# Performance work log

Hardware: AMD Instinct MI355X
Metric: run time of the kernel (lower is better)

Reference implementation:

```python
import jax, jax.numpy as jnp
import numpy as np

N, C, E = 100000, 128, 1600000


def setup_inputs() -> dict:
    key = jax.random.key(0)
    ks = jax.random.split(key, 7)
    s = 1.0 / np.sqrt(C)
    return {
        "x": jax.random.normal(ks[0], (N, C), jnp.float32),
        "edge_index": jax.random.randint(ks[1], (2, E), 0, N),
        "weight": jax.random.uniform(ks[2], (C, C), jnp.float32, -s, s),   # GCN weight (evolved)
        "w_ih": jax.random.uniform(ks[3], (4 * C, C), jnp.float32, -s, s),  # LSTM input weights
        "w_hh": jax.random.uniform(ks[4], (4 * C, C), jnp.float32, -s, s),  # LSTM hidden weights (h0=0 -> no fwd effect)
        "b_ih": jax.random.uniform(ks[5], (4 * C,), jnp.float32, -s, s),
        "b_hh": jax.random.uniform(ks[6], (4 * C,), jnp.float32, -s, s),
    }


def reference(x, edge_index, weight, w_ih, w_hh, b_ih, b_hh):
    n = x.shape[0]
    # --- LSTM single step over the weight matrix (seq=1, batch=C, h0=c0=0) ---
    # h0 = 0 so w_hh contributes nothing to the forward pass.
    gates = weight @ w_ih.T + b_ih + b_hh  # [C, 4C]
    i, f, g, o = jnp.split(gates, 4, axis=1)
    c = jax.nn.sigmoid(i) * jnp.tanh(g)           # f-gate * c0 = 0
    w_new = jax.nn.sigmoid(o) * jnp.tanh(c)       # evolved GCN weight [C, C]
    del w_hh  # zero forward contribution, kept for faithfulness

    xw = x @ w_new  # [N, C]
    loop = jnp.arange(n)
    src = jnp.concatenate([edge_index[0], loop])  # source j
    dst = jnp.concatenate([edge_index[1], loop])  # target i
    ew = jnp.ones(src.shape[0], x.dtype)          # edge_weight defaults to 1 (improved=False -> self-loop weight 1)
    deg = jax.ops.segment_sum(ew, dst, num_segments=n)
    dinv = jnp.where(deg > 0, jax.lax.rsqrt(jnp.maximum(deg, 1e-12)), 0.0)
    norm = dinv[src] * dinv[dst]                  # [E+N]
    # gather messages, scale, scatter-add to targets
    return jax.ops.segment_sum(xw[src] * norm[:, None], dst, num_segments=n)
```

## Files before the change

### kernel.cpp

```cpp
#include <hip/hip_runtime.h>
#include <hip/hip_bf16.h>
#include <math.h>

typedef __hip_bfloat16  bf16_t;
typedef __attribute__((ext_vector_type(8))) short  short8;
typedef __attribute__((ext_vector_type(4))) float  f32x4;
typedef __attribute__((ext_vector_type(4))) int    intv4;

#define CDIM 128
#define KCAP 32

static __device__ __forceinline__ float sigm(float x){ return 1.0f/(1.0f+__expf(-x)); }
static __device__ __forceinline__ float bflo(unsigned u){ return __builtin_bit_cast(float, u << 16); }
static __device__ __forceinline__ float bfhi(unsigned u){ return __builtin_bit_cast(float, u & 0xffff0000u); }
static __device__ __forceinline__ unsigned short f2bf_u(float f){
    __hip_bfloat16 h = __float2bfloat16(f);
    return __builtin_bit_cast(unsigned short, h);
}
static __device__ __forceinline__ unsigned packbf(float a, float b){
    return (unsigned)f2bf_u(a) | ((unsigned)f2bf_u(b) << 16);
}
static __device__ __forceinline__ short f2bf_s(float f){
    return (short)f2bf_u(f);
}

__global__ void k_lstm(const float* __restrict__ weight, const float* __restrict__ w_ih,
                       const float* __restrict__ b_ih,   const float* __restrict__ b_hh,
                       short* __restrict__ wfrag, int* __restrict__ zptr, int zcount){
    const int gtid = blockIdx.x*CDIM + threadIdx.x;
    for(int i = gtid; i < zcount; i += CDIM*CDIM) zptr[i] = 0;

    __shared__ float wrow[CDIM];
    const int r = blockIdx.x, j = threadIdx.x;
    wrow[j] = weight[r*CDIM + j];
    __syncthreads();
    const float4* wi = (const float4*)(w_ih + (size_t)j*CDIM);
    const float4* wg = (const float4*)(w_ih + (size_t)(2*CDIM + j)*CDIM);
    const float4* wo = (const float4*)(w_ih + (size_t)(3*CDIM + j)*CDIM);
    const float4* wr = (const float4*)wrow;
    float si = 0.f, sg = 0.f, so = 0.f;
    #pragma unroll 8
    for(int k = 0; k < CDIM/4; k++){
        float4 w4 = wr[k];
        float4 a = wi[k]; si += w4.x*a.x + w4.y*a.y + w4.z*a.z + w4.w*a.w;
        float4 b = wg[k]; sg += w4.x*b.x + w4.y*b.y + w4.z*b.z + w4.w*b.w;
        float4 c = wo[k]; so += w4.x*c.x + w4.y*c.y + w4.z*c.z + w4.w*c.w;
    }
    si += b_ih[j]        + b_hh[j];
    sg += b_ih[2*CDIM+j] + b_hh[2*CDIM+j];
    so += b_ih[3*CDIM+j] + b_hh[3*CDIM+j];
    float c  = sigm(si)*tanhf(sg);
    float wv = sigm(so)*tanhf(c);
    const int t = r >> 5, quad = (r >> 3) & 3, jj = r & 7;
    const int n0 = j >> 4, mm = j & 15;
    wfrag[((size_t)((t*8 + n0)*64 + quad*16 + mm))*8 + jj] = f2bf_s(wv);
}

__global__ __launch_bounds__(256) void k_fillcast(const int* __restrict__ src, const int* __restrict__ dst,
        int e, int* __restrict__ cnt, int* __restrict__ csr,
        int2* __restrict__ spill, int* __restrict__ spillc, int nper,
        const float* __restrict__ x, bf16_t* __restrict__ y0, int nf4,
        int castblocks, int edgeblocks){
    if((int)blockIdx.x < castblocks){
        const float4* xv = (const float4*)x;
        uint2* yv = (uint2*)y0;
        const int t0   = blockIdx.x*256 + threadIdx.x;
        const int step = castblocks*256;
        for(int i = t0; i < nf4; i += step){
            float4 v = xv[i];
            uint2 o; o.x = packbf(v.x, v.y); o.y = packbf(v.z, v.w);
            yv[i] = o;
        }
        return;
    }
    const int bid = (int)blockIdx.x - castblocks;
    const int grp = bid & 7;
    const int lo  = grp*nper, hi = lo + nper;
    const int tid = (bid >> 3)*256 + threadIdx.x;
    const int nt  = (edgeblocks >> 3)*256;
    const int e4  = e >> 2;
    const intv4* d4 = (const intv4*)dst;
    const intv4* s4 = (const intv4*)src;
    for(int i = tid; i < e4; i += nt){
        intv4 d = __builtin_nontemporal_load(d4 + i);
        intv4 s = __builtin_nontemporal_load(s4 + i);
        #pragma unroll
        for(int c = 0; c < 4; c++){
            int di = d[c];
            if(di >= lo && di < hi){
                int p = atomicAdd(&cnt[di], 1);
                if(p < KCAP) csr[(size_t)di*KCAP + p] = s[c];
                else { int sp = atomicAdd(spillc, 1); spill[sp] = make_int2(s[c], di); }
            }
        }
    }
    for(int k = e4*4 + tid; k < e; k += nt){
        int di = dst[k];
        if(di >= lo && di < hi){
            int sv = src[k];
            int p = atomicAdd(&cnt[di], 1);
            if(p < KCAP) csr[(size_t)di*KCAP + p] = sv;
            else { int sp = atomicAdd(spillc, 1); spill[sp] = make_int2(sv, di); }
        }
    }
}

__global__ __launch_bounds__(256) void k_agg(const bf16_t* __restrict__ y, const int* __restrict__ csr,
                      const int* __restrict__ deg, const int2* __restrict__ spill,
                      const int* __restrict__ spillc, bf16_t* __restrict__ agg, int n){
    const int node = (int)(((size_t)blockIdx.x*256 + threadIdx.x) >> 6);
    if(node >= n) return;
    const int lane = threadIdx.x & 63;
    const int q = lane >> 4, f = lane & 15;
    const int   cnt = deg[node];
    const float di  = rsqrtf((float)(cnt + 1));
    const int   m   = cnt < KCAP ? cnt : KCAP;
    const uint4* yrow = (const uint4*)y;
    uint4 sv = yrow[(size_t)node*16 + f];
    int jid = (lane < m) ? csr[(size_t)node*KCAP + lane] : 0;

    int jv[8];
    #pragma unroll
    for(int t = 0; t < 8; t++) jv[t] = __shfl(jid, 4*t + q, 64);

    int dgv[8];
    #pragma unroll
    for(int t = 0; t < 8; t++)
        if(4*t + q < m) dgv[t] = deg[jv[t]];

    uint4 v[8];
    #pragma unroll
    for(int t = 0; t < 8; t++)
        if(4*t + q < m) v[t] = yrow[(size_t)jv[t]*16 + f];

    float acc[8];
    #pragma unroll
    for(int i = 0; i < 8; i++) acc[i] = 0.f;
    #pragma unroll
    for(int t = 0; t < 8; t++){
        if(4*t + q < m){
            float dj = rsqrtf((float)(dgv[t] + 1));
            acc[0] += dj*bflo(v[t].x); acc[1] += dj*bfhi(v[t].x);
            acc[2] += dj*bflo(v[t].y); acc[3] += dj*bfhi(v[t].y);
            acc[4] += dj*bflo(v[t].z); acc[5] += dj*bfhi(v[t].z);
            acc[6] += dj*bflo(v[t].w); acc[7] += dj*bfhi(v[t].w);
        }
    }
    int sc = *spillc;
    if(sc > 0){
        for(int t = q; t < sc; t += 4){
            int2 sd = spill[t];
            if(sd.y == node){
                float dj = rsqrtf((float)(deg[sd.x] + 1));
                uint4 vv = yrow[(size_t)sd.x*16 + f];
                acc[0] += dj*bflo(vv.x); acc[1] += dj*bfhi(vv.x);
                acc[2] += dj*bflo(vv.y); acc[3] += dj*bfhi(vv.y);
                acc[4] += dj*bflo(vv.z); acc[5] += dj*bfhi(vv.z);
                acc[6] += dj*bflo(vv.w); acc[7] += dj*bfhi(vv.w);
            }
        }
    }
    #pragma unroll
    for(int i = 0; i < 8; i++){
        acc[i] += __shfl_xor(acc[i], 16, 64);
        acc[i] += __shfl_xor(acc[i], 32, 64);
    }
    if(q == 0){
        uint4 o;
        o.x = packbf(di*(acc[0] + di*bflo(sv.x)), di*(acc[1] + di*bfhi(sv.x)));
        o.y = packbf(di*(acc[2] + di*bflo(sv.y)), di*(acc[3] + di*bfhi(sv.y)));
        o.z = packbf(di*(acc[4] + di*bflo(sv.z)), di*(acc[5] + di*bfhi(sv.z)));
        o.w = packbf(di*(acc[6] + di*bflo(sv.w)), di*(acc[7] + di*bfhi(sv.w)));
        ((uint4*)agg)[(size_t)node*16 + f] = o;
    }
}

__global__ __launch_bounds__(256) void k_mgemm(const bf16_t* __restrict__ agg,
                                               const short* __restrict__ wfrag,
                                               float* __restrict__ out, int n){
    const int wid  = blockIdx.x*4 + (threadIdx.x >> 6);
    const int row0 = wid*16;
    if(row0 >= n) return;
    const int lane = threadIdx.x & 63;
    const int m    = lane & 15, quad = lane >> 4;
    int arow = row0 + m; if(arow > n-1) arow = n-1;
    const short* ap = (const short*)agg + (size_t)arow*CDIM + quad*8;
    short8 a0 = *(const short8*)(ap);
    short8 a1 = *(const short8*)(ap + 32);
    short8 a2 = *(const short8*)(ap + 64);
    short8 a3 = *(const short8*)(ap + 96);
    const short8* bp = (const short8*)wfrag;
    float* orow = out + (size_t)(row0 + quad*4)*CDIM + m;
    const bool full = (row0 + 16 <= n);
    #pragma unroll
    for(int n0 = 0; n0 < 8; n0++){
        f32x4 acc = {0.f, 0.f, 0.f, 0.f};
        acc = __builtin_amdgcn_mfma_f32_16x16x32_bf16(a0, bp[(0*8+n0)*64 + lane], acc, 0, 0, 0);
        acc = __builtin_amdgcn_mfma_f32_16x16x32_bf16(a1, bp[(1*8+n0)*64 + lane], acc, 0, 0, 0);
        acc = __builtin_amdgcn_mfma_f32_16x16x32_bf16(a2, bp[(2*8+n0)*64 + lane], acc, 0, 0, 0);
        acc = __builtin_amdgcn_mfma_f32_16x16x32_bf16(a3, bp[(3*8+n0)*64 + lane], acc, 0, 0, 0);
        if(full){
            #pragma unroll
            for(int r = 0; r < 4; r++)
                orow[(size_t)r*CDIM + n0*16] = acc[r];
        } else {
            #pragma unroll
            for(int r = 0; r < 4; r++)
                if(row0 + quad*4 + r < n) orow[(size_t)r*CDIM + n0*16] = acc[r];
        }
    }
}

extern "C" void kernel_launch(void* const* d_in, const int* in_sizes, int n_in,
                              void* d_out, int out_size, void* d_ws, size_t ws_size,
                              hipStream_t stream){
    const float* x      = (const float*)d_in[0];
    const int*   ei     = (const int*)  d_in[1];
    const float* weight = (const float*)d_in[2];
    const float* w_ih   = (const float*)d_in[3];
    const float* b_ih   = (const float*)d_in[5];
    const float* b_hh   = (const float*)d_in[6];
    float* out = (float*)d_out;

    const int n = in_sizes[0]/CDIM;
    const int e = in_sizes[1]/2;
    const int* srcp = ei;
    const int* dstp = ei + e;

    auto alignup = [](size_t v){ return (v + 255) & ~(size_t)255; };
    char*  base = (char*)d_ws;
    size_t o = 0;
    short*  wfrag  = (short*) (base+o); o += alignup((size_t)CDIM*CDIM*sizeof(short));
    int*    deg    = (int*)   (base+o); o += alignup((size_t)n*4);
    int*    spillc = (int*)   (base+o); o += alignup(256);
    size_t  zbytes = (size_t)((char*)(base+o) - (char*)deg);
    int*    csr    = (int*)   (base+o); o += alignup((size_t)n*KCAP*4);
    bf16_t* aggbuf = (bf16_t*)(base+o);

    bf16_t* y0    = (bf16_t*)d_out;
    int2*   spill = (int2*)((char*)d_out + (size_t)n*CDIM*sizeof(bf16_t));

    const int nper  = (n + 7)/8;
    const int castb = 512;
    const int edgeb = 1536;
    const int rb = (n + 3)/4;
    const int gw = (n + 15)/16;
    const int gb = (gw + 3)/4;

    k_lstm    <<<CDIM, CDIM, 0, stream>>>(weight, w_ih, b_ih, b_hh, wfrag,
                                          deg, (int)(zbytes/4));
    k_fillcast<<<castb+edgeb, 256, 0, stream>>>(srcp, dstp, e, deg, csr, spill, spillc, nper,
                                                x, y0, n*CDIM/4, castb, edgeb);
    k_agg     <<<rb, 256, 0, stream>>>(y0, csr, deg, spill, spillc, aggbuf, n);
    k_mgemm   <<<gb, 256, 0, stream>>>(aggbuf, wfrag, out, n);
}
```

Baseline: 277.2 us.

## Fuse aggregation and MFMA GEMM into one kernel via LDS staging

Merges the neighbor-aggregation kernel and the bf16 MFMA GEMM into one kernel. Each 1024-thread block aggregates 16 nodes into shared memory, and then 8 waves each compute one 16-column output tile. This removes the global round trip of the aggregated bf16 buffer and one launch. It also moves y0 and the spill list into the workspace, caps spill storage, lowers KCAP to 30, and raises the edge-fill block count. The tradeoffs are that half the waves idle during the GEMM phase and all waves must pass a block-wide barrier.

```diff
diff --git a/kernel.cpp b/kernel.cpp
--- a/kernel.cpp
+++ b/kernel.cpp
@@ -8,7 +8,8 @@
 typedef __attribute__((ext_vector_type(4))) int    intv4;
 
 #define CDIM 128
-#define KCAP 32
+#define KCAP 30
+#define SPILLCAP 65536
 
 static __device__ __forceinline__ float sigm(float x){ return 1.0f/(1.0f+__expf(-x)); }
 static __device__ __forceinline__ float bflo(unsigned u){ return __builtin_bit_cast(float, u << 16); }
@@ -90,7 +91,7 @@
             if(di >= lo && di < hi){
                 int p = atomicAdd(&cnt[di], 1);
                 if(p < KCAP) csr[(size_t)di*KCAP + p] = s[c];
-                else { int sp = atomicAdd(spillc, 1); spill[sp] = make_int2(s[c], di); }
+                else { int sp = atomicAdd(spillc, 1); if(sp < SPILLCAP) spill[sp] = make_int2(s[c], di); }
             }
         }
     }
@@ -100,63 +101,73 @@
             int sv = src[k];
             int p = atomicAdd(&cnt[di], 1);
             if(p < KCAP) csr[(size_t)di*KCAP + p] = sv;
-            else { int sp = atomicAdd(spillc, 1); spill[sp] = make_int2(sv, di); }
-        }
-    }
-}
-
-__global__ __launch_bounds__(256) void k_agg(const bf16_t* __restrict__ y, const int* __restrict__ csr,
-                      const int* __restrict__ deg, const int2* __restrict__ spill,
-                      const int* __restrict__ spillc, bf16_t* __restrict__ agg, int n){
-    const int node = (int)(((size_t)blockIdx.x*256 + threadIdx.x) >> 6);
-    if(node >= n) return;
+            else { int sp = atomicAdd(spillc, 1); if(sp < SPILLCAP) spill[sp] = make_int2(sv, di); }
+        }
+    }
+}
+
+__global__ __launch_bounds__(1024, 8) void k_aggmm(const bf16_t* __restrict__ y, const int* __restrict__ csr,
+        const int* __restrict__ deg, const int2* __restrict__ spill, const int* __restrict__ spillc,
+        const short* __restrict__ wfrag, float* __restrict__ out, int n){
+    __shared__ short alds[16][136];
+    const int wid  = threadIdx.x >> 6;
     const int lane = threadIdx.x & 63;
     const int q = lane >> 4, f = lane & 15;
-    const int   cnt = deg[node];
-    const float di  = rsqrtf((float)(cnt + 1));
-    const int   m   = cnt < KCAP ? cnt : KCAP;
+    const int base = blockIdx.x * 16;
+    const int node = base + wid;
     const uint4* yrow = (const uint4*)y;
-    uint4 sv = yrow[(size_t)node*16 + f];
-    int jid = (lane < m) ? csr[(size_t)node*KCAP + lane] : 0;
-
-    int jv[8];
-    #pragma unroll
-    for(int t = 0; t < 8; t++) jv[t] = __shfl(jid, 4*t + q, 64);
-
-    int dgv[8];
-    #pragma unroll
-    for(int t = 0; t < 8; t++)
-        if(4*t + q < m) dgv[t] = deg[jv[t]];
-
-    uint4 v[8];
-    #pragma unroll
-    for(int t = 0; t < 8; t++)
-        if(4*t + q < m) v[t] = yrow[(size_t)jv[t]*16 + f];
 
     float acc[8];
     #pragma unroll
     for(int i = 0; i < 8; i++) acc[i] = 0.f;
+    uint4 sv = make_uint4(0u,0u,0u,0u);
+    float di = 0.f;
+    int m = 0;
+    int jid = 0;
+    if(node < n){
+        const int cnt = deg[node];
+        di = rsqrtf((float)(cnt + 1));
+        m = cnt < KCAP ? cnt : KCAP;
+        sv = yrow[(size_t)node*16 + f];
+        jid = (lane < m) ? csr[(size_t)node*KCAP + lane] : 0;
+    }
     #pragma unroll
-    for(int t = 0; t < 8; t++){
-        if(4*t + q < m){
-            float dj = rsqrtf((float)(dgv[t] + 1));
-            acc[0] += dj*bflo(v[t].x); acc[1] += dj*bfhi(v[t].x);
-            acc[2] += dj*bflo(v[t].y); acc[3] += dj*bfhi(v[t].y);
-            acc[4] += dj*bflo(v[t].z); acc[5] += dj*bfhi(v[t].z);
-            acc[6] += dj*bflo(v[t].w); acc[7] += dj*bfhi(v[t].w);
-        }
-    }
-    int sc = *spillc;
-    if(sc > 0){
-        for(int t = q; t < sc; t += 4){
-            int2 sd = spill[t];
-            if(sd.y == node){
-                float dj = rsqrtf((float)(deg[sd.x] + 1));
-                uint4 vv = yrow[(size_t)sd.x*16 + f];
-                acc[0] += dj*bflo(vv.x); acc[1] += dj*bfhi(vv.x);
-                acc[2] += dj*bflo(vv.y); acc[3] += dj*bfhi(vv.y);
-                acc[4] += dj*bflo(vv.z); acc[5] += dj*bfhi(vv.z);
-                acc[6] += dj*bflo(vv.w); acc[7] += dj*bfhi(vv.w);
+    for(int half = 0; half < 2; half++){
+        const int kb = half*16;
+        if(kb < m){
+            int jv[4], dg[4]; uint4 v[4];
+            #pragma unroll
+            for(int t = 0; t < 4; t++) jv[t] = __shfl(jid, kb + 4*t + q, 64);
+            #pragma unroll
+            for(int t = 0; t < 4; t++) if(kb + 4*t + q < m) dg[t] = deg[jv[t]];
+            #pragma unroll
+            for(int t = 0; t < 4; t++) if(kb + 4*t + q < m) v[t] = yrow[(size_t)jv[t]*16 + f];
+            #pragma unroll
+            for(int t = 0; t < 4; t++){
+                if(kb + 4*t + q < m){
+                    float dj = rsqrtf((float)(dg[t] + 1));
+                    acc[0] += dj*bflo(v[t].x); acc[1] += dj*bfhi(v[t].x);
+                    acc[2] += dj*bflo(v[t].y); acc[3] += dj*bfhi(v[t].y);
+                    acc[4] += dj*bflo(v[t].z); acc[5] += dj*bfhi(v[t].z);
+                    acc[6] += dj*bflo(v[t].w); acc[7] += dj*bfhi(v[t].w);
+                }
+            }
+        }
+    }
+    if(node < n){
+        int sc = *spillc;
+        if(sc > 0){
+            if(sc > SPILLCAP) sc = SPILLCAP;
+            for(int t = q; t < sc; t += 4){
+                int2 sd = spill[t];
+                if(sd.y == node){
+                    float dj = rsqrtf((float)(deg[sd.x] + 1));
+                    uint4 vv = yrow[(size_t)sd.x*16 + f];
+                    acc[0] += dj*bflo(vv.x); acc[1] += dj*bfhi(vv.x);
+                    acc[2] += dj*bflo(vv.y); acc[3] += dj*bfhi(vv.y);
+                    acc[4] += dj*bflo(vv.z); acc[5] += dj*bfhi(vv.z);
+                    acc[6] += dj*bflo(vv.w); acc[7] += dj*bfhi(vv.w);
+                }
             }
         }
     }
@@ -171,43 +182,33 @@
         o.y = packbf(di*(acc[2] + di*bflo(sv.y)), di*(acc[3] + di*bfhi(sv.y)));
         o.z = packbf(di*(acc[4] + di*bflo(sv.z)), di*(acc[5] + di*bfhi(sv.z)));
         o.w = packbf(di*(acc[6] + di*bflo(sv.w)), di*(acc[7] + di*bfhi(sv.w)));
-        ((uint4*)agg)[(size_t)node*16 + f] = o;
-    }
-}
-
-__global__ __launch_bounds__(256) void k_mgemm(const bf16_t* __restrict__ agg,
-                                               const short* __restrict__ wfrag,
-                                               float* __restrict__ out, int n){
-    const int wid  = blockIdx.x*4 + (threadIdx.x >> 6);
-    const int row0 = wid*16;
-    if(row0 >= n) return;
-    const int lane = threadIdx.x & 63;
-    const int m    = lane & 15, quad = lane >> 4;
-    int arow = row0 + m; if(arow > n-1) arow = n-1;
-    const short* ap = (const short*)agg + (size_t)arow*CDIM + quad*8;
-    short8 a0 = *(const short8*)(ap);
-    short8 a1 = *(const short8*)(ap + 32);
-    short8 a2 = *(const short8*)(ap + 64);
-    short8 a3 = *(const short8*)(ap + 96);
+        *(uint4*)&alds[wid][f*8] = o;
+    }
+    __syncthreads();
+
+    if(wid >= 8) return;
+    const int mm = lane & 15, quad = lane >> 4;
+    short8 a0 = *(const short8*)&alds[mm][ 0 + quad*8];
+    short8 a1 = *(const short8*)&alds[mm][32 + quad*8];
+    short8 a2 = *(const short8*)&alds[mm][64 + quad*8];
+    short8 a3 = *(const short8*)&alds[mm][96 + quad*8];
     const short8* bp = (const short8*)wfrag;
-    float* orow = out + (size_t)(row0 + quad*4)*CDIM + m;
-    const bool full = (row0 + 16 <= n);
-    #pragma unroll
-    for(int n0 = 0; n0 < 8; n0++){
-        f32x4 acc = {0.f, 0.f, 0.f, 0.f};
-        acc = __builtin_amdgcn_mfma_f32_16x16x32_bf16(a0, bp[(0*8+n0)*64 + lane], acc, 0, 0, 0);
-        acc = __builtin_amdgcn_mfma_f32_16x16x32_bf16(a1, bp[(1*8+n0)*64 + lane], acc, 0, 0, 0);
-        acc = __builtin_amdgcn_mfma_f32_16x16x32_bf16(a2, bp[(2*8+n0)*64 + lane], acc, 0, 0, 0);
-        acc = __builtin_amdgcn_mfma_f32_16x16x32_bf16(a3, bp[(3*8+n0)*64 + lane], acc, 0, 0, 0);
-        if(full){
-            #pragma unroll
-            for(int r = 0; r < 4; r++)
-                orow[(size_t)r*CDIM + n0*16] = acc[r];
-        } else {
-            #pragma unroll
-            for(int r = 0; r < 4; r++)
-                if(row0 + quad*4 + r < n) orow[(size_t)r*CDIM + n0*16] = acc[r];
-        }
+    float* orow = out + (size_t)(base + quad*4)*CDIM + mm;
+    const bool full = (base + 16 <= n);
+    const int n0 = wid;
+    f32x4 accv = {0.f, 0.f, 0.f, 0.f};
+    accv = __builtin_amdgcn_mfma_f32_16x16x32_bf16(a0, bp[(0*8+n0)*64 + lane], accv, 0, 0, 0);
+    accv = __builtin_amdgcn_mfma_f32_16x16x32_bf16(a1, bp[(1*8+n0)*64 + lane], accv, 0, 0, 0);
+    accv = __builtin_amdgcn_mfma_f32_16x16x32_bf16(a2, bp[(2*8+n0)*64 + lane], accv, 0, 0, 0);
+    accv = __builtin_amdgcn_mfma_f32_16x16x32_bf16(a3, bp[(3*8+n0)*64 + lane], accv, 0, 0, 0);
+    if(full){
+        #pragma unroll
+        for(int r = 0; r < 4; r++)
+            orow[(size_t)r*CDIM + n0*16] = accv[r];
+    } else {
+        #pragma unroll
+        for(int r = 0; r < 4; r++)
+            if(base + quad*4 + r < n) orow[(size_t)r*CDIM + n0*16] = accv[r];
     }
 }
 
@@ -235,22 +236,17 @@
     int*    spillc = (int*)   (base+o); o += alignup(256);
     size_t  zbytes = (size_t)((char*)(base+o) - (char*)deg);
     int*    csr    = (int*)   (base+o); o += alignup((size_t)n*KCAP*4);
-    bf16_t* aggbuf = (bf16_t*)(base+o);
-
-    bf16_t* y0    = (bf16_t*)d_out;
-    int2*   spill = (int2*)((char*)d_out + (size_t)n*CDIM*sizeof(bf16_t));
+    bf16_t* y0     = (bf16_t*)(base+o); o += alignup((size_t)n*CDIM*sizeof(bf16_t));
+    int2*   spill  = (int2*)  (base+o); o += alignup((size_t)SPILLCAP*sizeof(int2));
 
     const int nper  = (n + 7)/8;
     const int castb = 512;
-    const int edgeb = 1536;
-    const int rb = (n + 3)/4;
-    const int gw = (n + 15)/16;
-    const int gb = (gw + 3)/4;
+    const int edgeb = 2048;
+    const int gb = (n + 15)/16;
 
     k_lstm    <<<CDIM, CDIM, 0, stream>>>(weight, w_ih, b_ih, b_hh, wfrag,
                                           deg, (int)(zbytes/4));
     k_fillcast<<<castb+edgeb, 256, 0, stream>>>(srcp, dstp, e, deg, csr, spill, spillc, nper,
                                                 x, y0, n*CDIM/4, castb, edgeb);
-    k_agg     <<<rb, 256, 0, stream>>>(y0, csr, deg, spill, spillc, aggbuf, n);
-    k_mgemm   <<<gb, 256, 0, stream>>>(aggbuf, wfrag, out, n);
-}
+    k_aggmm   <<<gb, 1024, 0, stream>>>(y0, csr, deg, spill, spillc, wfrag, out, n);
+}
```

Measured after the change: 310.1 us. 1.12x slower.
